# Optimization experiments

Hardware: AMD Instinct MI355X
Metric: run time of the kernel (lower is better)

The kernel has to match this reference:

```python
import jax, jax.numpy as jnp
import numpy as np
import math

WS = (8, 8)        # window_size
SHIFT = (4, 4)     # shift_size
HEADS = 12
C_DIM = 384


def _rel_position_bias(cpb_w1, cpb_b1, cpb_w2):
    ws0, ws1 = WS
    # continuous relative coords table, shape (2*ws0-1, 2*ws1-1, 2)
    ch = jnp.arange(-(ws0 - 1), ws0, dtype=jnp.float32)
    cw = jnp.arange(-(ws1 - 1), ws1, dtype=jnp.float32)
    table = jnp.stack(jnp.meshgrid(ch, cw, indexing='ij'), axis=-1)
    table = table / jnp.array([ws0 - 1, ws1 - 1], jnp.float32) * 8.0
    table = jnp.sign(table) * jnp.log2(jnp.abs(table) + 1.0) / 3.0
    # cpb MLP: 2 -> 512 -> HEADS (no bias on second layer)
    h = jax.nn.relu(table @ cpb_w1.T + cpb_b1)
    bias_table = (h @ cpb_w2.T).reshape(-1, HEADS)  # ((2ws0-1)*(2ws1-1), H)
    # static relative position index (numpy, shapes are static)
    coords = np.stack(np.meshgrid(np.arange(ws0), np.arange(ws1), indexing='ij'))
    coords = coords.reshape(2, -1)
    rel = (coords[:, :, None] - coords[:, None, :]).transpose(1, 2, 0)
    rel[..., 0] += ws0 - 1
    rel[..., 1] += ws1 - 1
    rel[..., 0] *= 2 * ws1 - 1
    idx = jnp.asarray(rel.sum(-1))  # (L, L)
    bias = bias_table[idx]          # (L, L, HEADS)
    bias = jnp.transpose(bias, (2, 0, 1))  # (HEADS, L, L)
    return 16.0 * jax.nn.sigmoid(bias)


def _shift_attn_mask(pad_H, pad_W):
    ws0, ws1 = WS
    s0, s1 = SHIFT
    m = np.zeros((pad_H, pad_W), dtype=np.float32)
    cnt = 0
    h_slices = ((0, pad_H - ws0), (pad_H - ws0, pad_H - s0), (pad_H - s0, pad_H))
    w_slices = ((0, pad_W - ws1), (pad_W - ws1, pad_W - s1), (pad_W - s1, pad_W))
    for h0, h1 in h_slices:
        for w0, w1 in w_slices:
            m[h0:h1, w0:w1] = cnt
            cnt += 1
    m = m.reshape(pad_H // ws0, ws0, pad_W // ws1, ws1)
    m = m.transpose(0, 2, 1, 3).reshape(-1, ws0 * ws1)  # (nW, L)
    diff = m[:, None, :] - m[:, :, None]
    mask = np.where(diff != 0, -100.0, 0.0).astype(np.float32)
    return jnp.asarray(mask)  # (nW, L, L)


def setup_inputs() -> dict:
    key = jax.random.key(0)
    ks = jax.random.split(key, 7)
    C = C_DIM
    x = jax.random.normal(ks[0], (16, 64, 64, C), jnp.float32)
    qkv_w = jax.random.normal(ks[1], (3 * C, C), jnp.float32) * 0.02
    qkv_b = jax.random.normal(ks[2], (3 * C,), jnp.float32) * 0.02
    proj_w = jax.random.normal(ks[3], (C, C), jnp.float32) * 0.02
    proj_b = jax.random.normal(ks[4], (C,), jnp.float32) * 0.02
    logit_scale = jnp.full((HEADS, 1, 1), math.log(10.0), jnp.float32)
    cpb_w1 = jax.random.normal(ks[5], (512, 2), jnp.float32) * 0.02
    cpb_b1 = jnp.zeros((512,), jnp.float32)
    cpb_w2 = jax.random.normal(ks[6], (HEADS, 512), jnp.float32) * 0.02
    return {"x": x, "qkv_w": qkv_w, "qkv_b": qkv_b, "proj_w": proj_w,
            "proj_b": proj_b, "logit_scale": logit_scale,
            "cpb_w1": cpb_w1, "cpb_b1": cpb_b1, "cpb_w2": cpb_w2}


def reference(x, qkv_w, qkv_b, proj_w, proj_b, logit_scale, cpb_w1, cpb_b1, cpb_w2):
    B, H, W, C = x.shape
    ws0, ws1 = WS
    s0, s1 = SHIFT
    L = ws0 * ws1
    hd = C // HEADS
    # H, W are divisible by window -> no padding; shift stays nonzero
    bias = _rel_position_bias(cpb_w1, cpb_b1, cpb_w2)  # (HEADS, L, L)
    xr = jnp.roll(x, (-s0, -s1), axis=(1, 2))
    nWh, nWw = H // ws0, W // ws1
    nW = nWh * nWw
    # window partition -> (B*nW, L, C)
    xw = xr.reshape(B, nWh, ws0, nWw, ws1, C).transpose(0, 1, 3, 2, 4, 5)
    xw = xw.reshape(B * nW, L, C)
    # qkv with the k-bias zeroed (SwinV2 convention)
    qb = qkv_b.at[C:2 * C].set(0.0)
    qkv = xw @ qkv_w.T + qb
    qkv = qkv.reshape(B * nW, L, 3, HEADS, hd).transpose(2, 0, 3, 1, 4)
    q, k, v = qkv[0], qkv[1], qkv[2]  # each (B*nW, HEADS, L, hd)
    # cosine attention
    qn = q / jnp.maximum(jnp.linalg.norm(q, axis=-1, keepdims=True), 1e-12)
    kn = k / jnp.maximum(jnp.linalg.norm(k, axis=-1, keepdims=True), 1e-12)
    scale = jnp.exp(jnp.minimum(logit_scale, math.log(100.0)))  # (HEADS,1,1)
    attn = jnp.einsum('whid,whjd->whij', qn, kn) * scale + bias
    # shifted-window mask
    mask = _shift_attn_mask(H, W)  # (nW, L, L)
    attn = attn.reshape(B, nW, HEADS, L, L) + mask[None, :, None]
    attn = jax.nn.softmax(attn.reshape(B * nW, HEADS, L, L), axis=-1)
    out = jnp.einsum('whij,whjd->whid', attn, v)
    out = out.transpose(0, 2, 1, 3).reshape(B * nW, L, C)
    out = out @ proj_w.T + proj_b
    # window reverse
    out = out.reshape(B, nWh, nWw, ws0, ws1, C).transpose(0, 1, 3, 2, 4, 5)
    out = out.reshape(B, H, W, C)
    out = jnp.roll(out, (s0, s1), axis=(1, 2))
    return out
```

## Files before the change

### kernel.cpp

```cpp
#include <hip/hip_runtime.h>
#include <cstdint>
#include <cstddef>

typedef unsigned short u16;
typedef __attribute__((ext_vector_type(8))) short s16x8;
typedef __attribute__((ext_vector_type(4))) float f32x4;

#define DEV static __device__ __forceinline__

constexpr int C = 384;
constexpr int HEADS = 12;
constexpr int NQKV = 3 * C;
constexpr int TOK = 16 * 64 * 64;

constexpr size_t OFF_QKVW = 0;
constexpr size_t OFF_PROJW = OFF_QKVW + (size_t)NQKV * C * 2;
constexpr size_t OFF_BIAS  = OFF_PROJW + (size_t)C * C * 2;
constexpr size_t OFF_XG    = OFF_BIAS + (size_t)HEADS * 64 * 64 * 4;
constexpr size_t OFF_QN    = OFF_XG + (size_t)TOK * C * 2;
constexpr size_t OFF_KN    = OFF_QN + (size_t)TOK * C * 2;
constexpr size_t OFF_VT    = OFF_KN + (size_t)TOK * C * 2;
constexpr size_t OFF_MLP   = OFF_VT + (size_t)TOK * C * 2;
constexpr size_t OFF_AO    = OFF_XG;

DEV u16 f2bf(float f) {
  union { float f; uint32_t u; } v; v.f = f;
  uint32_t r = v.u + 0x7FFFu + ((v.u >> 16) & 1u);
  return (u16)(r >> 16);
}

DEV float bf2f(short h) {
  union { uint32_t u; float f; } v; v.u = ((uint32_t)(u16)h) << 16;
  return v.f;
}

DEV void async16(const u16* g, u16* l) {
  __builtin_amdgcn_global_load_lds((const __attribute__((address_space(1))) uint32_t*)g,
                                   (__attribute__((address_space(3))) uint32_t*)l, 16, 0, 0);
}

__global__ __launch_bounds__(256) void prep_kernel(
    const float* __restrict__ x, const float* __restrict__ qkv_w,
    const float* __restrict__ proj_w, u16* __restrict__ wq,
    u16* __restrict__ wp, u16* __restrict__ xg) {
  int idx = blockIdx.x * 256 + threadIdx.x;
  constexpr int QW = NQKV * C / 8;
  constexpr int PW = C * C / 8;
  const float* src;
  u16* dst;
  if (idx < QW) {
    src = qkv_w + (size_t)idx * 8; dst = wq + (size_t)idx * 8;
  } else if (idx < QW + PW) {
    int i = idx - QW;
    src = proj_w + (size_t)i * 8; dst = wp + (size_t)i * 8;
  } else {
    int i = idx - QW - PW;
    int r = i / 48, c8 = i % 48;
    int b = r >> 12, w = (r >> 6) & 63, t = r & 63;
    int y  = ((w >> 3) * 8 + (t >> 3) + 4) & 63;
    int xc = ((w & 7) * 8 + (t & 7) + 4) & 63;
    src = x + (((size_t)(b * 64 + y)) * 64 + xc) * C + c8 * 8;
    dst = xg + (size_t)r * C + (size_t)c8 * 8;
  }
  float4 a = ((const float4*)src)[0];
  float4 bq = ((const float4*)src)[1];
  union { u16 h[8]; uint4 v; } o;
  o.h[0] = f2bf(a.x);  o.h[1] = f2bf(a.y);  o.h[2] = f2bf(a.z);  o.h[3] = f2bf(a.w);
  o.h[4] = f2bf(bq.x); o.h[5] = f2bf(bq.y); o.h[6] = f2bf(bq.z); o.h[7] = f2bf(bq.w);
  *(uint4*)dst = o.v;
}

__global__ __launch_bounds__(256) void bias_mlp_kernel(
    const float* __restrict__ w1, const float* __restrict__ b1,
    const float* __restrict__ w2, float* __restrict__ mlp_out) {
  const int gid = blockIdx.x * 256 + threadIdx.x;
  if (gid >= 225 * 12) return;
  const int pt = gid / 12, q = gid % 12;
  const int a = pt / 15, b = pt % 15;
  const float dy = (float)(a - 7) * (8.f / 7.f);
  const float dx = (float)(b - 7) * (8.f / 7.f);
  const float t0 = copysignf(log2f(fabsf(dy) + 1.f) * (1.f / 3.f), dy);
  const float t1 = copysignf(log2f(fabsf(dx) + 1.f) * (1.f / 3.f), dx);
  float acc = 0.f;
  for (int j = 0; j < 512; ++j) {
    const float hh = fmaxf(w1[2 * j] * t0 + w1[2 * j + 1] * t1 + b1[j], 0.f);
    acc += hh * w2[q * 512 + j];
  }
  mlp_out[gid] = acc;
}

__global__ __launch_bounds__(256) void bias_expand_kernel(
    const float* __restrict__ mlp_out, float* __restrict__ biasf) {
  const int o = blockIdx.x * 256 + threadIdx.x;
  const int j = o & 63, i = (o >> 6) & 63, h = o >> 12;
  const int e = ((i >> 3) - (j >> 3) + 7) * 15 + ((i & 7) - (j & 7) + 7);
  const float v = mlp_out[e * 12 + h];
  biasf[o] = 16.f / (1.f + __expf(-v));
}

__global__ __launch_bounds__(512, 2) void qkv_kernel(
    const u16* __restrict__ xg, const u16* __restrict__ wq,
    const float* __restrict__ qkv_b,
    u16* __restrict__ qn, u16* __restrict__ kn, u16* __restrict__ vt) {
  __shared__ __attribute__((aligned(16))) u16 smem[4][128 * 64];
  const int tid = threadIdx.x, lane = tid & 63, wid = tid >> 6;
  const int l15 = lane & 15, qrt = lane >> 4;
  const int bid = blockIdx.x;
  const int swz = (bid & 7) * 576 + (bid >> 3);
  const int n_blk = swz % 9, m_blk = swz / 9;
  const int m0 = m_blk * 128, n0 = n_blk * 128;
  const int wm = wid & 3, wn = wid >> 2;

  auto stage = [&](int buf, int t) {
    const int k0 = t * 64;
    #pragma unroll
    for (int it = 0; it < 2; ++it) {
      const int c = it * 512 + tid;
      const int r = c >> 3;
      const int g = (c & 7) ^ (r & 7);
      async16(xg + (size_t)(m0 + r) * C + k0 + g * 8, &smem[buf][c * 8]);
      async16(wq + (size_t)(n0 + r) * C + k0 + g * 8, &smem[2 + buf][c * 8]);
    }
  };
  auto ldfrag = [&](const u16* base, int row, int g) -> s16x8 {
    return *(const s16x8*)((const char*)base + row * 128 + ((g ^ (row & 7)) * 16));
  };

  f32x4 acc[2][4];
  #pragma unroll
  for (int i = 0; i < 2; ++i)
    #pragma unroll
    for (int j = 0; j < 4; ++j) acc[i][j] = f32x4{0.f, 0.f, 0.f, 0.f};

  stage(0, 0);
  for (int t = 0; t < 6; ++t) {
    const int buf = t & 1;
    asm volatile("s_waitcnt vmcnt(0)" ::: "memory");
    __syncthreads();
    if (t < 5) stage(buf ^ 1, t + 1);
    s16x8 af[2][2], bf[2][4];
    #pragma unroll
    for (int kk = 0; kk < 2; ++kk) {
      const int g = kk * 4 + qrt;
      #pragma unroll
      for (int mi = 0; mi < 2; ++mi)
        af[kk][mi] = ldfrag(smem[buf], wm * 32 + mi * 16 + l15, g);
      #pragma unroll
      for (int ni = 0; ni < 4; ++ni)
        bf[kk][ni] = ldfrag(smem[2 + buf], wn * 64 + ni * 16 + l15, g);
    }
    #pragma unroll
    for (int kk = 0; kk < 2; ++kk)
      #pragma unroll
      for (int mi = 0; mi < 2; ++mi)
        #pragma unroll
        for (int ni = 0; ni < 4; ++ni)
          acc[mi][ni] = __builtin_amdgcn_mfma_f32_16x16x32_bf16(af[kk][mi], bf[kk][ni], acc[mi][ni], 0, 0, 0);
  }

  const int sec = n0 / C;
  const int colbase = n0 + wn * 64;
  float qb[4];
  #pragma unroll
  for (int ni = 0; ni < 4; ++ni)
    qb[ni] = (sec == 1) ? 0.f : qkv_b[colbase + ni * 16 + l15];

  if (sec < 2) {
    u16* const base = (sec == 0) ? qn : kn;
    const int hb = (colbase % C) >> 5;
    #pragma unroll
    for (int mi = 0; mi < 2; ++mi) {
      #pragma unroll
      for (int r = 0; r < 4; ++r) {
        const int grow = m0 + wm * 32 + mi * 16 + qrt * 4 + r;
        const int w = grow >> 6, t_ = grow & 63;
        u16* dst0 = base + ((size_t)(w * 12 + hb) * 64 + t_) * 32 + l15;
        u16* dst1 = base + ((size_t)(w * 12 + hb + 1) * 64 + t_) * 32 + l15;
        dst0[0]  = f2bf(acc[mi][0][r] + qb[0]);
        dst0[16] = f2bf(acc[mi][1][r] + qb[1]);
        dst1[0]  = f2bf(acc[mi][2][r] + qb[2]);
        dst1[16] = f2bf(acc[mi][3][r] + qb[3]);
      }
    }
  } else {
    __syncthreads();
    u16* tr = &smem[0][0] + wid * 2048;
    #pragma unroll
    for (int ni = 0; ni < 4; ++ni) {
      const int dl = ni * 16 + l15;
      #pragma unroll
      for (int mi = 0; mi < 2; ++mi) {
        const int t0 = mi * 16 + qrt * 4;
        union { u16 h[4]; uint2 u; } pk;
        #pragma unroll
        for (int r = 0; r < 4; ++r) pk.h[r] = f2bf(acc[mi][ni][r] + qb[ni]);
        const int byte = dl * 64 + (((t0 >> 2) ^ (dl & 7)) << 3);
        *(uint2*)((char*)tr + byte) = pk.u;
      }
    }
    const int w_ = (m0 + wm * 32) >> 6;
    const int tbase = (wm & 1) * 32;
    const int hbase = (colbase % C) >> 5;
    #pragma unroll
    for (int i = 0; i < 8; ++i) {
      const int d = i * 8 + (lane >> 3);
      const int ck = lane & 7;
      const int byte = d * 64 + ((ck ^ (d & 7)) << 3);
      const uint2 val = *(const uint2*)((const char*)tr + byte);
      const int head = hbase + (d >> 5), din = d & 31;
      *(uint2*)(vt + (((size_t)(w_ * 12 + head) * 32 + din) * 64 + tbase + ck * 4)) = val;
    }
  }
}

__global__ __launch_bounds__(256, 4) void attn_kernel(
    const u16* __restrict__ qn, const u16* __restrict__ kn, const u16* __restrict__ vt,
    const float* __restrict__ ls, const float* __restrict__ biasf, u16* __restrict__ ao) {
  __shared__ __attribute__((aligned(16))) u16 strip_s[4][4096];
  const int tid = threadIdx.x, lane = tid & 63, wv = tid >> 6;
  char* strip = (char*)strip_s[wv];
  const int gid = blockIdx.x * 4 + wv;
  const int w = gid / 12, h = gid - w * 12;
  const int win = w & 63, wy = win >> 3, wx = win & 7;
  const int l15 = lane & 15, qrt = lane >> 4;
  const f32x4 z4 = {0.f, 0.f, 0.f, 0.f};

  const u16* qh = qn + (size_t)gid * 2048;
  const u16* kh = kn + (size_t)gid * 2048;
  const u16* vh = vt + (size_t)gid * 2048;
  const float sc = __expf(fminf(ls[h], 4.605170185988091f));

  s16x8 aq[4], bk[4];
  #pragma unroll
  for (int mi = 0; mi < 4; ++mi)
    aq[mi] = *(const s16x8*)(qh + (mi * 16 + l15) * 32 + qrt * 8);
  #pragma unroll
  for (int ni = 0; ni < 4; ++ni)
    bk[ni] = *(const s16x8*)(kh + (ni * 16 + l15) * 32 + qrt * 8);
  #pragma unroll
  for (int mi = 0; mi < 4; ++mi) {
    float f[8]; float ss = 0.f;
    #pragma unroll
    for (int e = 0; e < 8; ++e) { f[e] = bf2f(aq[mi][e]); ss = fmaf(f[e], f[e], ss); }
    ss += __shfl_xor(ss, 16); ss += __shfl_xor(ss, 32);
    const float rn = sc / fmaxf(sqrtf(ss), 1e-12f);
    #pragma unroll
    for (int e = 0; e < 8; ++e) aq[mi][e] = (short)f2bf(f[e] * rn);
  }
  #pragma unroll
  for (int ni = 0; ni < 4; ++ni) {
    float f[8]; float ss = 0.f;
    #pragma unroll
    for (int e = 0; e < 8; ++e) { f[e] = bf2f(bk[ni][e]); ss = fmaf(f[e], f[e], ss); }
    ss += __shfl_xor(ss, 16); ss += __shfl_xor(ss, 32);
    const float rn = 1.f / fmaxf(sqrtf(ss), 1e-12f);
    #pragma unroll
    for (int e = 0; e < 8; ++e) bk[ni][e] = (short)f2bf(f[e] * rn);
  }

  f32x4 acc[4][4];
  #pragma unroll
  for (int mi = 0; mi < 4; ++mi)
    #pragma unroll
    for (int ni = 0; ni < 4; ++ni)
      acc[mi][ni] = __builtin_amdgcn_mfma_f32_16x16x32_bf16(aq[mi], bk[ni], z4, 0, 0, 0);

  int ccls[4];
  #pragma unroll
  for (int ni = 0; ni < 4; ++ni) {
    const int j = ni * 16 + l15;
    const int gy = wy * 8 + (j >> 3), gx = wx * 8 + (j & 7);
    ccls[ni] = ((gy < 56 ? 0 : (gy < 60 ? 1 : 2)) << 2) | (gx < 56 ? 0 : (gx < 60 ? 1 : 2));
  }

  #pragma unroll
  for (int mi = 0; mi < 4; ++mi) {
    #pragma unroll
    for (int r = 0; r < 4; ++r) {
      const int i = mi * 16 + qrt * 4 + r;
      const int gy = wy * 8 + (i >> 3), gx = wx * 8 + (i & 7);
      const int rcl = ((gy < 56 ? 0 : (gy < 60 ? 1 : 2)) << 2) | (gx < 56 ? 0 : (gx < 60 ? 1 : 2));
      const float* brow = biasf + ((h << 6) + i) * 64 + l15;
      float mx = -3e38f;
      #pragma unroll
      for (int ni = 0; ni < 4; ++ni) {
        float val = acc[mi][ni][r] + brow[ni * 16];
        if (rcl != ccls[ni]) val -= 100.f;
        acc[mi][ni][r] = val;
        mx = fmaxf(mx, val);
      }
      mx = fmaxf(mx, __shfl_xor(mx, 1));
      mx = fmaxf(mx, __shfl_xor(mx, 2));
      mx = fmaxf(mx, __shfl_xor(mx, 4));
      mx = fmaxf(mx, __shfl_xor(mx, 8));
      float sum = 0.f;
      #pragma unroll
      for (int ni = 0; ni < 4; ++ni) {
        const float pv = __expf(acc[mi][ni][r] - mx);
        acc[mi][ni][r] = pv; sum += pv;
      }
      sum += __shfl_xor(sum, 1); sum += __shfl_xor(sum, 2);
      sum += __shfl_xor(sum, 4); sum += __shfl_xor(sum, 8);
      const float inv = 1.f / sum;
      #pragma unroll
      for (int ni = 0; ni < 4; ++ni) {
        const int j2 = (ni * 16 + l15) * 2;
        *(u16*)(strip + i * 128 + (j2 ^ ((i & 7) << 4))) = f2bf(acc[mi][ni][r] * inv);
      }
    }
  }

  s16x8 pa[4][2];
  #pragma unroll
  for (int ni2 = 0; ni2 < 4; ++ni2) {
    const int t = ni2 * 16 + l15;
    #pragma unroll
    for (int kk = 0; kk < 2; ++kk) {
      const int j2 = (kk * 32 + qrt * 8) * 2;
      pa[ni2][kk] = *(const s16x8*)(strip + t * 128 + (j2 ^ ((t & 7) << 4)));
    }
  }
  f32x4 o2[2][4];
  #pragma unroll
  for (int mi2 = 0; mi2 < 2; ++mi2) {
    #pragma unroll
    for (int ni2 = 0; ni2 < 4; ++ni2) o2[mi2][ni2] = z4;
    #pragma unroll
    for (int kk = 0; kk < 2; ++kk) {
      const s16x8 va = *(const s16x8*)(vh + (mi2 * 16 + l15) * 64 + kk * 32 + qrt * 8);
      #pragma unroll
      for (int ni2 = 0; ni2 < 4; ++ni2)
        o2[mi2][ni2] = __builtin_amdgcn_mfma_f32_16x16x32_bf16(va, pa[ni2][kk], o2[mi2][ni2], 0, 0, 0);
    }
  }
  #pragma unroll
  for (int mi2 = 0; mi2 < 2; ++mi2) {
    #pragma unroll
    for (int ni2 = 0; ni2 < 4; ++ni2) {
      const int t = ni2 * 16 + l15;
      #pragma unroll
      for (int rp = 0; rp < 2; ++rp) {
        const int d0 = mi2 * 16 + qrt * 4 + rp * 2;
        union { u16 h2[2]; uint32_t u; } pk;
        pk.h2[0] = f2bf(o2[mi2][ni2][rp * 2]);
        pk.h2[1] = f2bf(o2[mi2][ni2][rp * 2 + 1]);
        *(uint32_t*)(strip + t * 128 + ((d0 * 2) ^ ((t & 7) << 4))) = pk.u;
      }
    }
  }
  u16* aob = ao + ((size_t)h * TOK + (size_t)w * 64) * 32;
  #pragma unroll
  for (int it = 0; it < 4; ++it) {
    const int t = (lane >> 2) + it * 16, g = lane & 3;
    const uint4 val = *(const uint4*)(strip + t * 128 + ((g * 16) ^ ((t & 7) << 4)));
    *(uint4*)(aob + (size_t)t * 32 + g * 8) = val;
  }
}

__global__ __launch_bounds__(512, 2) void proj_kernel(
    const u16* __restrict__ ao, const u16* __restrict__ pw,
    const float* __restrict__ proj_b, float* __restrict__ out) {
  __shared__ __attribute__((aligned(16))) u16 smem[4][128 * 64];
  const int tid = threadIdx.x, lane = tid & 63, wid = tid >> 6;
  const int l15 = lane & 15, qrt = lane >> 4;
  const int bid = blockIdx.x;
  const int swz = (bid & 7) * 192 + (bid >> 3);
  const int n_blk = swz % 3, m_blk = swz / 3;
  const int m0 = m_blk * 128, n0 = n_blk * 128;
  const int wm = wid & 3, wn = wid >> 2;

  auto stage = [&](int buf, int t) {
    #pragma unroll
    for (int it = 0; it < 2; ++it) {
      const int c = it * 512 + tid;
      const int r = c >> 3;
      const int g = (c & 7) ^ (r & 7);
      const int p = t * 2 + (g >> 2);
      async16(ao + ((size_t)p * TOK + (m0 + r)) * 32 + (g & 3) * 8, &smem[buf][c * 8]);
      async16(pw + (size_t)(n0 + r) * C + t * 64 + g * 8, &smem[2 + buf][c * 8]);
    }
  };
  auto ldfrag = [&](const u16* base, int row, int g) -> s16x8 {
    return *(const s16x8*)((const char*)base + row * 128 + ((g ^ (row & 7)) * 16));
  };

  f32x4 acc[2][4];
  #pragma unroll
  for (int i = 0; i < 2; ++i)
    #pragma unroll
    for (int j = 0; j < 4; ++j) acc[i][j] = f32x4{0.f, 0.f, 0.f, 0.f};

  stage(0, 0);
  for (int t = 0; t < 6; ++t) {
    const int buf = t & 1;
    asm volatile("s_waitcnt vmcnt(0)" ::: "memory");
    __syncthreads();
    if (t < 5) stage(buf ^ 1, t + 1);
    s16x8 af[2][2], bf[2][4];
    #pragma unroll
    for (int kk = 0; kk < 2; ++kk) {
      const int g = kk * 4 + qrt;
      #pragma unroll
      for (int mi = 0; mi < 2; ++mi)
        af[kk][mi] = ldfrag(smem[buf], wm * 32 + mi * 16 + l15, g);
      #pragma unroll
      for (int ni = 0; ni < 4; ++ni)
        bf[kk][ni] = ldfrag(smem[2 + buf], wn * 64 + ni * 16 + l15, g);
    }
    #pragma unroll
    for (int kk = 0; kk < 2; ++kk)
      #pragma unroll
      for (int mi = 0; mi < 2; ++mi)
        #pragma unroll
        for (int ni = 0; ni < 4; ++ni)
          acc[mi][ni] = __builtin_amdgcn_mfma_f32_16x16x32_bf16(af[kk][mi], bf[kk][ni], acc[mi][ni], 0, 0, 0);
  }

  #pragma unroll
  for (int ni = 0; ni < 4; ++ni) {
    const int n = n0 + wn * 64 + ni * 16 + l15;
    const float pb = proj_b[n];
    #pragma unroll
    for (int mi = 0; mi < 2; ++mi) {
      #pragma unroll
      for (int r = 0; r < 4; ++r) {
        const int grow = m0 + wm * 32 + mi * 16 + qrt * 4 + r;
        const int bimg = grow >> 12, win = (grow >> 6) & 63, t_ = grow & 63;
        const int y = ((win >> 3) * 8 + (t_ >> 3) + 4) & 63;
        const int xc = ((win & 7) * 8 + (t_ & 7) + 4) & 63;
        out[(((size_t)bimg * 64 + y) * 64 + xc) * C + n] = acc[mi][ni][r] + pb;
      }
    }
  }
}

extern "C" void kernel_launch(void* const* d_in, const int* in_sizes, int n_in,
                              void* d_out, int out_size, void* d_ws, size_t ws_size,
                              hipStream_t stream) {
  const float* x           = (const float*)d_in[0];
  const float* qkv_w       = (const float*)d_in[1];
  const float* qkv_b       = (const float*)d_in[2];
  const float* proj_w      = (const float*)d_in[3];
  const float* proj_b      = (const float*)d_in[4];
  const float* logit_scale = (const float*)d_in[5];
  const float* cpb_w1      = (const float*)d_in[6];
  const float* cpb_b1      = (const float*)d_in[7];
  const float* cpb_w2      = (const float*)d_in[8];
  char* ws = (char*)d_ws;
  u16* qkvwb  = (u16*)(ws + OFF_QKVW);
  u16* projwb = (u16*)(ws + OFF_PROJW);
  float* biasf = (float*)(ws + OFF_BIAS);
  u16* xg = (u16*)(ws + OFF_XG);
  u16* qn = (u16*)(ws + OFF_QN);
  u16* kn = (u16*)(ws + OFF_KN);
  u16* vt = (u16*)(ws + OFF_VT);
  float* mlp = (float*)(ws + OFF_MLP);
  u16* ao = (u16*)(ws + OFF_AO);

  prep_kernel<<<12576, 256, 0, stream>>>(x, qkv_w, proj_w, qkvwb, projwb, xg);
  bias_mlp_kernel<<<11, 256, 0, stream>>>(cpb_w1, cpb_b1, cpb_w2, mlp);
  bias_expand_kernel<<<192, 256, 0, stream>>>(mlp, biasf);
  qkv_kernel<<<4608, 512, 0, stream>>>(xg, qkvwb, qkv_b, qn, kn, vt);
  attn_kernel<<<3072, 256, 0, stream>>>(qn, kn, vt, logit_scale, biasf, ao);
  proj_kernel<<<1536, 512, 0, stream>>>(ao, projwb, proj_b, (float*)d_out);
}
```

Measured before the change: 206.0 us.

## Triple-buffer QKV GEMM with K-step 32 and raise occupancy hint

```diff
diff --git a/kernel.cpp b/kernel.cpp
--- a/kernel.cpp
+++ b/kernel.cpp
@@ -98,11 +98,11 @@
   biasf[o] = 16.f / (1.f + __expf(-v));
 }
 
-__global__ __launch_bounds__(512, 2) void qkv_kernel(
+__global__ __launch_bounds__(512, 6) void qkv_kernel(
     const u16* __restrict__ xg, const u16* __restrict__ wq,
     const float* __restrict__ qkv_b,
     u16* __restrict__ qn, u16* __restrict__ kn, u16* __restrict__ vt) {
-  __shared__ __attribute__((aligned(16))) u16 smem[4][128 * 64];
+  __shared__ __attribute__((aligned(16))) u16 smem[6][128 * 32];
   const int tid = threadIdx.x, lane = tid & 63, wid = tid >> 6;
   const int l15 = lane & 15, qrt = lane >> 4;
   const int bid = blockIdx.x;
@@ -112,18 +112,19 @@
   const int wm = wid & 3, wn = wid >> 2;
 
   auto stage = [&](int buf, int t) {
-    const int k0 = t * 64;
-    #pragma unroll
-    for (int it = 0; it < 2; ++it) {
-      const int c = it * 512 + tid;
-      const int r = c >> 3;
-      const int g = (c & 7) ^ (r & 7);
-      async16(xg + (size_t)(m0 + r) * C + k0 + g * 8, &smem[buf][c * 8]);
-      async16(wq + (size_t)(n0 + r) * C + k0 + g * 8, &smem[2 + buf][c * 8]);
-    }
+    const int k0 = t * 32;
+    const int c = tid;
+    const int rr = c >> 3;
+    const int qx = (c & 7) ^ (rr & 7);
+    const int r = (rr << 1) + (qx >> 2);
+    const int g = qx & 3;
+    async16(xg + (size_t)(m0 + r) * C + k0 + g * 8, &smem[buf][c * 8]);
+    async16(wq + (size_t)(n0 + r) * C + k0 + g * 8, &smem[3 + buf][c * 8]);
   };
   auto ldfrag = [&](const u16* base, int row, int g) -> s16x8 {
-    return *(const s16x8*)((const char*)base + row * 128 + ((g ^ (row & 7)) * 16));
+    const int rr = row >> 1;
+    const int pos = (((row & 1) << 2) + g) ^ (rr & 7);
+    return *(const s16x8*)((const char*)base + rr * 128 + pos * 16);
   };
 
   f32x4 acc[2][4];
@@ -133,29 +134,26 @@
     for (int j = 0; j < 4; ++j) acc[i][j] = f32x4{0.f, 0.f, 0.f, 0.f};
 
   stage(0, 0);
-  for (int t = 0; t < 6; ++t) {
-    const int buf = t & 1;
-    asm volatile("s_waitcnt vmcnt(0)" ::: "memory");
-    __syncthreads();
-    if (t < 5) stage(buf ^ 1, t + 1);
-    s16x8 af[2][2], bf[2][4];
-    #pragma unroll
-    for (int kk = 0; kk < 2; ++kk) {
-      const int g = kk * 4 + qrt;
-      #pragma unroll
-      for (int mi = 0; mi < 2; ++mi)
-        af[kk][mi] = ldfrag(smem[buf], wm * 32 + mi * 16 + l15, g);
+  stage(1, 1);
+  for (int t = 0; t < 12; ++t) {
+    const int buf = t % 3;
+    if (t < 11) asm volatile("s_waitcnt vmcnt(2) lgkmcnt(0)" ::: "memory");
+    else        asm volatile("s_waitcnt vmcnt(0) lgkmcnt(0)" ::: "memory");
+    __builtin_amdgcn_s_barrier();
+    if (t < 10) stage((t + 2) % 3, t + 2);
+    s16x8 af[2], bf[4];
+    const int g = qrt;
+    #pragma unroll
+    for (int mi = 0; mi < 2; ++mi)
+      af[mi] = ldfrag(smem[buf], wm * 32 + mi * 16 + l15, g);
+    #pragma unroll
+    for (int ni = 0; ni < 4; ++ni)
+      bf[ni] = ldfrag(smem[3 + buf], wn * 64 + ni * 16 + l15, g);
+    #pragma unroll
+    for (int mi = 0; mi < 2; ++mi)
       #pragma unroll
       for (int ni = 0; ni < 4; ++ni)
-        bf[kk][ni] = ldfrag(smem[2 + buf], wn * 64 + ni * 16 + l15, g);
-    }
-    #pragma unroll
-    for (int kk = 0; kk < 2; ++kk)
-      #pragma unroll
-      for (int mi = 0; mi < 2; ++mi)
-        #pragma unroll
-        for (int ni = 0; ni < 4; ++ni)
-          acc[mi][ni] = __builtin_amdgcn_mfma_f32_16x16x32_bf16(af[kk][mi], bf[kk][ni], acc[mi][ni], 0, 0, 0);
+        acc[mi][ni] = __builtin_amdgcn_mfma_f32_16x16x32_bf16(af[mi], bf[ni], acc[mi][ni], 0, 0, 0);
   }
 
   const int sec = n0 / C;
```

Measured after the change: 217.0 us. +5.3%, slower.

## Enlarge QKV GEMM tile to 128x384 so each block computes a full Q/K/V section

Applied to the files above, without the earlier changes.

```diff
diff --git a/kernel.cpp b/kernel.cpp
--- a/kernel.cpp
+++ b/kernel.cpp
@@ -102,35 +102,45 @@
     const u16* __restrict__ xg, const u16* __restrict__ wq,
     const float* __restrict__ qkv_b,
     u16* __restrict__ qn, u16* __restrict__ kn, u16* __restrict__ vt) {
-  __shared__ __attribute__((aligned(16))) u16 smem[4][128 * 64];
+  extern __shared__ __attribute__((aligned(16))) u16 smem[];
   const int tid = threadIdx.x, lane = tid & 63, wid = tid >> 6;
   const int l15 = lane & 15, qrt = lane >> 4;
   const int bid = blockIdx.x;
-  const int swz = (bid & 7) * 576 + (bid >> 3);
-  const int n_blk = swz % 9, m_blk = swz / 9;
-  const int m0 = m_blk * 128, n0 = n_blk * 128;
-  const int wm = wid & 3, wn = wid >> 2;
+  const int swz = (bid & 7) * 192 + (bid >> 3);
+  const int n_blk = swz % 3, m_blk = swz / 3;
+  const int m0 = m_blk * 128;
+  const int sec = n_blk;
+  const int n0 = n_blk * C;
+  const int wm = wid & 1, wn = wid >> 1;
 
   auto stage = [&](int buf, int t) {
     const int k0 = t * 64;
+    u16* abuf = smem + buf * 8192;
+    u16* bbuf = smem + 16384 + buf * 24576;
     #pragma unroll
     for (int it = 0; it < 2; ++it) {
       const int c = it * 512 + tid;
       const int r = c >> 3;
       const int g = (c & 7) ^ (r & 7);
-      async16(xg + (size_t)(m0 + r) * C + k0 + g * 8, &smem[buf][c * 8]);
-      async16(wq + (size_t)(n0 + r) * C + k0 + g * 8, &smem[2 + buf][c * 8]);
+      async16(xg + (size_t)(m0 + r) * C + k0 + g * 8, abuf + c * 8);
+    }
+    #pragma unroll
+    for (int it = 0; it < 6; ++it) {
+      const int c = it * 512 + tid;
+      const int r = c >> 3;
+      const int g = (c & 7) ^ (r & 7);
+      async16(wq + (size_t)(n0 + r) * C + k0 + g * 8, bbuf + c * 8);
     }
   };
   auto ldfrag = [&](const u16* base, int row, int g) -> s16x8 {
     return *(const s16x8*)((const char*)base + row * 128 + ((g ^ (row & 7)) * 16));
   };
 
-  f32x4 acc[2][4];
-  #pragma unroll
-  for (int i = 0; i < 2; ++i)
-    #pragma unroll
-    for (int j = 0; j < 4; ++j) acc[i][j] = f32x4{0.f, 0.f, 0.f, 0.f};
+  f32x4 acc[4][6];
+  #pragma unroll
+  for (int i = 0; i < 4; ++i)
+    #pragma unroll
+    for (int j = 0; j < 6; ++j) acc[i][j] = f32x4{0.f, 0.f, 0.f, 0.f};
 
   stage(0, 0);
   for (int t = 0; t < 6; ++t) {
@@ -138,77 +148,75 @@
     asm volatile("s_waitcnt vmcnt(0)" ::: "memory");
     __syncthreads();
     if (t < 5) stage(buf ^ 1, t + 1);
-    s16x8 af[2][2], bf[2][4];
+    const u16* abuf = smem + buf * 8192;
+    const u16* bbuf = smem + 16384 + buf * 24576;
+    s16x8 af[2][4], bf[2][6];
     #pragma unroll
     for (int kk = 0; kk < 2; ++kk) {
       const int g = kk * 4 + qrt;
       #pragma unroll
-      for (int mi = 0; mi < 2; ++mi)
-        af[kk][mi] = ldfrag(smem[buf], wm * 32 + mi * 16 + l15, g);
-      #pragma unroll
-      for (int ni = 0; ni < 4; ++ni)
-        bf[kk][ni] = ldfrag(smem[2 + buf], wn * 64 + ni * 16 + l15, g);
+      for (int mi = 0; mi < 4; ++mi)
+        af[kk][mi] = ldfrag(abuf, wm * 64 + mi * 16 + l15, g);
+      #pragma unroll
+      for (int ni = 0; ni < 6; ++ni)
+        bf[kk][ni] = ldfrag(bbuf, wn * 96 + ni * 16 + l15, g);
     }
     #pragma unroll
     for (int kk = 0; kk < 2; ++kk)
       #pragma unroll
-      for (int mi = 0; mi < 2; ++mi)
+      for (int mi = 0; mi < 4; ++mi)
         #pragma unroll
-        for (int ni = 0; ni < 4; ++ni)
+        for (int ni = 0; ni < 6; ++ni)
           acc[mi][ni] = __builtin_amdgcn_mfma_f32_16x16x32_bf16(af[kk][mi], bf[kk][ni], acc[mi][ni], 0, 0, 0);
   }
 
-  const int sec = n0 / C;
-  const int colbase = n0 + wn * 64;
-  float qb[4];
-  #pragma unroll
-  for (int ni = 0; ni < 4; ++ni)
-    qb[ni] = (sec == 1) ? 0.f : qkv_b[colbase + ni * 16 + l15];
+  float qb[6];
+  #pragma unroll
+  for (int ni = 0; ni < 6; ++ni)
+    qb[ni] = (sec == 1) ? 0.f : qkv_b[n0 + wn * 96 + ni * 16 + l15];
 
   if (sec < 2) {
     u16* const base = (sec == 0) ? qn : kn;
-    const int hb = (colbase % C) >> 5;
-    #pragma unroll
-    for (int mi = 0; mi < 2; ++mi) {
-      #pragma unroll
-      for (int r = 0; r < 4; ++r) {
-        const int grow = m0 + wm * 32 + mi * 16 + qrt * 4 + r;
-        const int w = grow >> 6, t_ = grow & 63;
-        u16* dst0 = base + ((size_t)(w * 12 + hb) * 64 + t_) * 32 + l15;
-        u16* dst1 = base + ((size_t)(w * 12 + hb + 1) * 64 + t_) * 32 + l15;
-        dst0[0]  = f2bf(acc[mi][0][r] + qb[0]);
-        dst0[16] = f2bf(acc[mi][1][r] + qb[1]);
-        dst1[0]  = f2bf(acc[mi][2][r] + qb[2]);
-        dst1[16] = f2bf(acc[mi][3][r] + qb[3]);
+    #pragma unroll
+    for (int p = 0; p < 3; ++p) {
+      const int hb = wn * 3 + p;
+      #pragma unroll
+      for (int mi = 0; mi < 4; ++mi) {
+        #pragma unroll
+        for (int r = 0; r < 4; ++r) {
+          const int grow = m0 + wm * 64 + mi * 16 + qrt * 4 + r;
+          const int w = grow >> 6, t_ = grow & 63;
+          u16* dst = base + ((size_t)(w * 12 + hb) * 64 + t_) * 32 + l15;
+          dst[0]  = f2bf(acc[mi][2 * p][r]     + qb[2 * p]);
+          dst[16] = f2bf(acc[mi][2 * p + 1][r] + qb[2 * p + 1]);
+        }
       }
     }
   } else {
     __syncthreads();
-    u16* tr = &smem[0][0] + wid * 2048;
-    #pragma unroll
-    for (int ni = 0; ni < 4; ++ni) {
+    u16* tr = smem + wid * 6144;
+    #pragma unroll
+    for (int ni = 0; ni < 6; ++ni) {
       const int dl = ni * 16 + l15;
       #pragma unroll
-      for (int mi = 0; mi < 2; ++mi) {
-        const int t0 = mi * 16 + qrt * 4;
+      for (int mi = 0; mi < 4; ++mi) {
+        const int tg = mi * 4 + qrt;
         union { u16 h[4]; uint2 u; } pk;
         #pragma unroll
         for (int r = 0; r < 4; ++r) pk.h[r] = f2bf(acc[mi][ni][r] + qb[ni]);
-        const int byte = dl * 64 + (((t0 >> 2) ^ (dl & 7)) << 3);
+        const int byte = dl * 128 + ((tg ^ (dl & 7)) << 3);
         *(uint2*)((char*)tr + byte) = pk.u;
       }
     }
-    const int w_ = (m0 + wm * 32) >> 6;
-    const int tbase = (wm & 1) * 32;
-    const int hbase = (colbase % C) >> 5;
-    #pragma unroll
-    for (int i = 0; i < 8; ++i) {
-      const int d = i * 8 + (lane >> 3);
-      const int ck = lane & 7;
-      const int byte = d * 64 + ((ck ^ (d & 7)) << 3);
+    const int w_ = (m0 + wm * 64) >> 6;
+    #pragma unroll
+    for (int i = 0; i < 24; ++i) {
+      const int dl = i * 4 + (lane >> 4);
+      const int tg = lane & 15;
+      const int byte = dl * 128 + ((tg ^ (dl & 7)) << 3);
       const uint2 val = *(const uint2*)((const char*)tr + byte);
-      const int head = hbase + (d >> 5), din = d & 31;
-      *(uint2*)(vt + (((size_t)(w_ * 12 + head) * 32 + din) * 64 + tbase + ck * 4)) = val;
+      const int head = wn * 3 + (dl >> 5), din = dl & 31;
+      *(uint2*)(vt + (((size_t)(w_ * 12 + head) * 32 + din) * 64 + tg * 4)) = val;
     }
   }
 }
@@ -457,10 +465,13 @@
   float* mlp = (float*)(ws + OFF_MLP);
   u16* ao = (u16*)(ws + OFF_AO);
 
+  hipFuncSetAttribute((const void*)qkv_kernel,
+                      hipFuncAttributeMaxDynamicSharedMemorySize, 131072);
+
   prep_kernel<<<12576, 256, 0, stream>>>(x, qkv_w, proj_w, qkvwb, projwb, xg);
   bias_mlp_kernel<<<11, 256, 0, stream>>>(cpb_w1, cpb_b1, cpb_w2, mlp);
   bias_expand_kernel<<<192, 256, 0, stream>>>(mlp, biasf);
-  qkv_kernel<<<4608, 512, 0, stream>>>(xg, qkvwb, qkv_b, qn, kn, vt);
+  qkv_kernel<<<1536, 512, 131072, stream>>>(xg, qkvwb, qkv_b, qn, kn, vt);
   attn_kernel<<<3072, 256, 0, stream>>>(qn, kn, vt, logit_scale, biasf, ao);
   proj_kernel<<<1536, 512, 0, stream>>>(ao, projwb, proj_b, (float*)d_out);
 }
```

After: 208.9 us. No clear change (+1.4%).
